# Kernel tuning notes

Measured on AMD Instinct MI355X. Metric: run time of the kernel, lower is better.

The kernel has to match this reference:

```python
import jax, jax.numpy as jnp
import numpy as np

BATCH = 262144
CLUSTER = 100

def _boost_generators():
    # Standard Lorentz boost generators K_x, K_y, K_z (symmetric, metric (+,-,-,-)).
    K = np.zeros((3, 4, 4), dtype=np.float32)
    for j in range(3):
        K[j, 0, j + 1] = 1.0
        K[j, j + 1, 0] = 1.0
    return jnp.asarray(K)

def setup_inputs() -> dict:
    key = jax.random.key(0)
    k1, k2, k3, k4 = jax.random.split(key, 4)
    T = jax.random.normal(k1, (BATCH, CLUSTER, 4), dtype=jnp.float32)
    # build() initializes boosts/bias uniform[0,1) scaled by 0.33 (|b| < 1 => gamma real)
    Bo = jax.random.uniform(k2, (CLUSTER, 3), dtype=jnp.float32) * 0.33
    Bi = jax.random.uniform(k3, (1, 3), dtype=jnp.float32) * 0.33
    W = jax.random.uniform(k4, (CLUSTER, 1), dtype=jnp.float32)
    K_mats = _boost_generators()
    return {"T": T, "Bo": Bo, "Bi": Bi, "W": W, "K_mats": K_mats}

def _lorentz(x, boosts, K_mats, weights=None):
    # x: (batch, C, 4), boosts: (C, 3) -> (batch, 4)
    mag = jnp.sqrt(jnp.sum(boosts * boosts, axis=1, keepdims=True))  # (C,1)
    n = boosts / mag                                                  # (C,3)
    g = 1.0 / jnp.sqrt(1.0 - mag * mag)                               # (C,1) gamma
    nK = jnp.einsum('cj,jad->cad', n, K_mats)                         # (C,4,4)
    nK2 = jnp.einsum('cab,cbd->cad', nK, nK)                          # (C,4,4)
    B = (jnp.eye(4, dtype=x.dtype)[None]
         - (g * mag)[..., None] * nK
         + (g - 1.0)[..., None] * nK2)                                # (C,4,4)
    if weights is not None:
        B = weights[:, :, None] * B                                   # per-element scalar weight
    # sum over cluster of B_c @ x[:, c]
    return jnp.einsum('cad,bcd->ba', B, x)

def reference(T, Bo, Bi, W, K_mats):
    summed = _lorentz(T, Bo, K_mats, weights=W)            # (batch, 4)
    out = _lorentz(summed[:, None, :], Bi, K_mats)         # (batch, 4)
    return out.reshape(T.shape[0], 1, 4)
```

## Files before the change

kernel.cpp:

```cpp
#include <hip/hip_runtime.h>
#include <math.h>

#define BATCH   262144
#define CLUSTER 100

__device__ inline void boost_mat(float bx, float by, float bz, float B[4][4]) {
    float m2  = bx * bx + by * by + bz * bz;
    float mag = sqrtf(m2);
    float nx = bx / mag, ny = by / mag, nz = bz / mag;
    float g  = 1.0f / sqrtf(1.0f - mag * mag);
    float gm = g * mag;
    float gm1 = g - 1.0f;
    float n[3] = {nx, ny, nz};
    B[0][0] = 1.0f + gm1 * (nx * nx + ny * ny + nz * nz);
    for (int j = 0; j < 3; ++j) {
        B[0][j + 1] = -gm * n[j];
        B[j + 1][0] = -gm * n[j];
    }
    for (int i = 0; i < 3; ++i)
        for (int j = 0; j < 3; ++j)
            B[i + 1][j + 1] = ((i == j) ? 1.0f : 0.0f) + gm1 * n[i] * n[j];
}

#define DOT4(mm, vv) ((mm).x*(vv).x + (mm).y*(vv).y + (mm).z*(vv).z + (mm).w*(vv).w)

__global__ __launch_bounds__(256) void lorentz_fused_kernel(
        const float* __restrict__ T,
        const float* __restrict__ Bo,
        const float* __restrict__ Bi,
        const float* __restrict__ W,
        float* __restrict__ out) {
    __shared__ float sMr[4][CLUSTER * 4];

    int tid  = threadIdx.x;
    int wave = tid >> 6;
    int lane = tid & 63;
    int q = lane & 15;
    int g = lane >> 4;
    long long base = (long long)blockIdx.x * 64 + wave * 16;

    const float* P0 = T + (base + g +  0) * (CLUSTER * 4);
    const float* P1 = T + (base + g +  4) * (CLUSTER * 4);
    const float* P2 = T + (base + g +  8) * (CLUSTER * 4);
    const float* P3 = T + (base + g + 12) * (CLUSTER * 4);

    float4 v0 = *(const float4*)(P0 + q * 4);
    float4 v1 = *(const float4*)(P1 + q * 4);
    float4 v2 = *(const float4*)(P2 + q * 4);
    float4 v3 = *(const float4*)(P3 + q * 4);

    if (tid < CLUSTER) {
        float BiM[4][4], BoM[4][4];
        boost_mat(Bi[0], Bi[1], Bi[2], BiM);
        boost_mat(Bo[tid * 3 + 0], Bo[tid * 3 + 1], Bo[tid * 3 + 2], BoM);
        float w = W[tid];
        for (int a = 0; a < 4; ++a)
            for (int d = 0; d < 4; ++d) {
                float s = 0.0f;
                for (int e = 0; e < 4; ++e)
                    s += BiM[a][e] * (w * BoM[e][d]);
                sMr[a][tid * 4 + d] = s;
            }
    }
    __syncthreads();

    float4 a0 = {0.f, 0.f, 0.f, 0.f};
    float4 a1 = a0, a2 = a0, a3 = a0;

    #define ACCSTEP(c)                                                        \
    {                                                                         \
        float4 m0 = *(const float4*)&sMr[0][(c) * 4];                         \
        float4 m1 = *(const float4*)&sMr[1][(c) * 4];                         \
        float4 m2 = *(const float4*)&sMr[2][(c) * 4];                         \
        float4 m3 = *(const float4*)&sMr[3][(c) * 4];                         \
        a0.x += DOT4(m0, v0); a0.y += DOT4(m1, v0); a0.z += DOT4(m2, v0); a0.w += DOT4(m3, v0); \
        a1.x += DOT4(m0, v1); a1.y += DOT4(m1, v1); a1.z += DOT4(m2, v1); a1.w += DOT4(m3, v1); \
        a2.x += DOT4(m0, v2); a2.y += DOT4(m1, v2); a2.z += DOT4(m2, v2); a2.w += DOT4(m3, v2); \
        a3.x += DOT4(m0, v3); a3.y += DOT4(m1, v3); a3.z += DOT4(m2, v3); a3.w += DOT4(m3, v3); \
    }

    for (int t = 0; t < 6; ++t) {
        int c = 16 * t + q;
        ACCSTEP(c)
        if (t < 5) {
            int cn = c + 16;
            v0 = *(const float4*)(P0 + cn * 4);
            v1 = *(const float4*)(P1 + cn * 4);
            v2 = *(const float4*)(P2 + cn * 4);
            v3 = *(const float4*)(P3 + cn * 4);
        } else if (q < 4) {
            int cn = 96 + q;
            v0 = *(const float4*)(P0 + cn * 4);
            v1 = *(const float4*)(P1 + cn * 4);
            v2 = *(const float4*)(P2 + cn * 4);
            v3 = *(const float4*)(P3 + cn * 4);
        }
    }
    if (q < 4) {
        ACCSTEP(96 + q)
    }
    #undef ACCSTEP

    #define RED(f) f += __shfl_xor(f, 1); f += __shfl_xor(f, 2); \
                   f += __shfl_xor(f, 4); f += __shfl_xor(f, 8);
    RED(a0.x) RED(a0.y) RED(a0.z) RED(a0.w)
    RED(a1.x) RED(a1.y) RED(a1.z) RED(a1.w)
    RED(a2.x) RED(a2.y) RED(a2.z) RED(a2.w)
    RED(a3.x) RED(a3.y) RED(a3.z) RED(a3.w)
    #undef RED

    float4 o = a0;
    if (q == 1) o = a1;
    if (q == 2) o = a2;
    if (q == 3) o = a3;
    if (q < 4)
        ((float4*)out)[base + g + 4 * q] = o;
}

extern "C" void kernel_launch(void* const* d_in, const int* in_sizes, int n_in,
                              void* d_out, int out_size, void* d_ws, size_t ws_size,
                              hipStream_t stream) {
    const float* T  = (const float*)d_in[0];
    const float* Bo = (const float*)d_in[1];
    const float* Bi = (const float*)d_in[2];
    const float* W  = (const float*)d_in[3];

    float* out = (float*)d_out;

    int blocks = BATCH / 64;
    lorentz_fused_kernel<<<blocks, 256, 0, stream>>>(T, Bo, Bi, W, out);
}
```

Measured before the change: 82.90 us.

## Stage input rows through shared memory with coalesced bulk loads

Each wave now loads its 8 contiguous input rows with fully coalesced float4 loads into registers, then writes them to shared memory. The dot products are computed from shared memory after the block barrier. Each block now handles 32 rows instead of 64, with 2 rows per 16-lane group. This is meant to increase memory-level parallelism and coalescing on the bandwidth-bound read of T, at the cost of large shared-memory use that can limit occupancy and of an extra LDS round trip.

```diff
diff --git a/kernel.cpp b/kernel.cpp
--- a/kernel.cpp
+++ b/kernel.cpp
@@ -24,77 +24,74 @@
 
 #define DOT4(mm, vv) ((mm).x*(vv).x + (mm).y*(vv).y + (mm).z*(vv).z + (mm).w*(vv).w)
 
-__global__ __launch_bounds__(256) void lorentz_fused_kernel(
-        const float* __restrict__ T,
-        const float* __restrict__ Bo,
-        const float* __restrict__ Bi,
-        const float* __restrict__ W,
-        float* __restrict__ out) {
-    __shared__ float sMr[4][CLUSTER * 4];
+__global__ __launch_bounds__(256) void lorentz_staged_kernel(
+        const float4* __restrict__ T4,
+        const float*  __restrict__ Bo,
+        const float*  __restrict__ Bi,
+        const float*  __restrict__ W,
+        float4* __restrict__ out4) {
+    __shared__ float  sMr[4][CLUSTER * 4];
+    __shared__ float4 sT[4][800];
 
     int tid  = threadIdx.x;
-    int wave = tid >> 6;
+    int w    = tid >> 6;
     int lane = tid & 63;
-    int q = lane & 15;
-    int g = lane >> 4;
-    long long base = (long long)blockIdx.x * 64 + wave * 16;
 
-    const float* P0 = T + (base + g +  0) * (CLUSTER * 4);
-    const float* P1 = T + (base + g +  4) * (CLUSTER * 4);
-    const float* P2 = T + (base + g +  8) * (CLUSTER * 4);
-    const float* P3 = T + (base + g + 12) * (CLUSTER * 4);
+    long long waveRow = (long long)blockIdx.x * 32 + w * 8;
+    const float4* src = T4 + waveRow * CLUSTER;
 
-    float4 v0 = *(const float4*)(P0 + q * 4);
-    float4 v1 = *(const float4*)(P1 + q * 4);
-    float4 v2 = *(const float4*)(P2 + q * 4);
-    float4 v3 = *(const float4*)(P3 + q * 4);
+    float4 r[13];
+    #pragma unroll
+    for (int s = 0; s < 12; ++s)
+        r[s] = src[s * 64 + lane];
+    if (lane < 32)
+        r[12] = src[768 + lane];
 
     if (tid < CLUSTER) {
         float BiM[4][4], BoM[4][4];
         boost_mat(Bi[0], Bi[1], Bi[2], BiM);
         boost_mat(Bo[tid * 3 + 0], Bo[tid * 3 + 1], Bo[tid * 3 + 2], BoM);
-        float w = W[tid];
+        float wt = W[tid];
         for (int a = 0; a < 4; ++a)
             for (int d = 0; d < 4; ++d) {
                 float s = 0.0f;
                 for (int e = 0; e < 4; ++e)
-                    s += BiM[a][e] * (w * BoM[e][d]);
+                    s += BiM[a][e] * (wt * BoM[e][d]);
                 sMr[a][tid * 4 + d] = s;
             }
     }
+
+    #pragma unroll
+    for (int s = 0; s < 12; ++s)
+        sT[w][s * 64 + lane] = r[s];
+    if (lane < 32)
+        sT[w][768 + lane] = r[12];
+
     __syncthreads();
 
+    int q = lane & 15;
+    int g = lane >> 4;
+    const float4* row0 = &sT[w][(2 * g)     * CLUSTER];
+    const float4* row1 = &sT[w][(2 * g + 1) * CLUSTER];
+
     float4 a0 = {0.f, 0.f, 0.f, 0.f};
-    float4 a1 = a0, a2 = a0, a3 = a0;
+    float4 a1 = a0;
 
     #define ACCSTEP(c)                                                        \
     {                                                                         \
+        float4 v0 = row0[c], v1 = row1[c];                                    \
         float4 m0 = *(const float4*)&sMr[0][(c) * 4];                         \
         float4 m1 = *(const float4*)&sMr[1][(c) * 4];                         \
         float4 m2 = *(const float4*)&sMr[2][(c) * 4];                         \
         float4 m3 = *(const float4*)&sMr[3][(c) * 4];                         \
         a0.x += DOT4(m0, v0); a0.y += DOT4(m1, v0); a0.z += DOT4(m2, v0); a0.w += DOT4(m3, v0); \
         a1.x += DOT4(m0, v1); a1.y += DOT4(m1, v1); a1.z += DOT4(m2, v1); a1.w += DOT4(m3, v1); \
-        a2.x += DOT4(m0, v2); a2.y += DOT4(m1, v2); a2.z += DOT4(m2, v2); a2.w += DOT4(m3, v2); \
-        a3.x += DOT4(m0, v3); a3.y += DOT4(m1, v3); a3.z += DOT4(m2, v3); a3.w += DOT4(m3, v3); \
     }
 
+    #pragma unroll
     for (int t = 0; t < 6; ++t) {
         int c = 16 * t + q;
         ACCSTEP(c)
-        if (t < 5) {
-            int cn = c + 16;
-            v0 = *(const float4*)(P0 + cn * 4);
-            v1 = *(const float4*)(P1 + cn * 4);
-            v2 = *(const float4*)(P2 + cn * 4);
-            v3 = *(const float4*)(P3 + cn * 4);
-        } else if (q < 4) {
-            int cn = 96 + q;
-            v0 = *(const float4*)(P0 + cn * 4);
-            v1 = *(const float4*)(P1 + cn * 4);
-            v2 = *(const float4*)(P2 + cn * 4);
-            v3 = *(const float4*)(P3 + cn * 4);
-        }
     }
     if (q < 4) {
         ACCSTEP(96 + q)
@@ -105,28 +102,22 @@
                    f += __shfl_xor(f, 4); f += __shfl_xor(f, 8);
     RED(a0.x) RED(a0.y) RED(a0.z) RED(a0.w)
     RED(a1.x) RED(a1.y) RED(a1.z) RED(a1.w)
-    RED(a2.x) RED(a2.y) RED(a2.z) RED(a2.w)
-    RED(a3.x) RED(a3.y) RED(a3.z) RED(a3.w)
     #undef RED
 
-    float4 o = a0;
-    if (q == 1) o = a1;
-    if (q == 2) o = a2;
-    if (q == 3) o = a3;
-    if (q < 4)
-        ((float4*)out)[base + g + 4 * q] = o;
+    if (q == 0) out4[waveRow + 2 * g]     = a0;
+    if (q == 1) out4[waveRow + 2 * g + 1] = a1;
 }
 
 extern "C" void kernel_launch(void* const* d_in, const int* in_sizes, int n_in,
                               void* d_out, int out_size, void* d_ws, size_t ws_size,
                               hipStream_t stream) {
-    const float* T  = (const float*)d_in[0];
-    const float* Bo = (const float*)d_in[1];
-    const float* Bi = (const float*)d_in[2];
-    const float* W  = (const float*)d_in[3];
+    const float4* T4 = (const float4*)d_in[0];
+    const float*  Bo = (const float*)d_in[1];
+    const float*  Bi = (const float*)d_in[2];
+    const float*  W  = (const float*)d_in[3];
 
-    float* out = (float*)d_out;
+    float4* out4 = (float4*)d_out;
 
-    int blocks = BATCH / 64;
-    lorentz_fused_kernel<<<blocks, 256, 0, stream>>>(T, Bo, Bi, W, out);
+    int blocks = BATCH / 32;
+    lorentz_staged_kernel<<<blocks, 256, 0, stream>>>(T4, Bo, Bi, W, out4);
 }
```

Result: slower. 171.4 us (+106.7%).
